# Kernel optimization log

Hardware: AMD Instinct MI355X
Metric: run time of the kernel (lower is better)

## Reference

```python
import jax, jax.numpy as jnp
import numpy as np
import math

D_MODEL = 1024
NHEAD = 16
D_K = D_MODEL // NHEAD
LAMDA_ATT = 1.0
B, L = 2, 2048


def setup_inputs() -> dict:
    key = jax.random.key(0)
    ks = jax.random.split(key, 10)
    s = 1.0 / math.sqrt(D_MODEL)
    x = jax.random.normal(ks[0], (B, L, D_MODEL), dtype=jnp.float32)
    delta_r = jax.random.uniform(ks[1], (B, L), dtype=jnp.float32)  # positive, fed to log
    Wq = jax.random.normal(ks[2], (D_MODEL, D_MODEL), dtype=jnp.float32) * s
    Wk = jax.random.normal(ks[3], (D_MODEL, D_MODEL), dtype=jnp.float32) * s
    Wv = jax.random.normal(ks[4], (D_MODEL, D_MODEL), dtype=jnp.float32) * s
    Wo = jax.random.normal(ks[5], (D_MODEL, D_MODEL), dtype=jnp.float32) * s
    bq = jnp.zeros((D_MODEL,), jnp.float32)
    bk = jnp.zeros((D_MODEL,), jnp.float32)
    bv = jnp.zeros((D_MODEL,), jnp.float32)
    bo = jnp.zeros((D_MODEL,), jnp.float32)
    return {"x": x, "delta_r": delta_r, "Wq": Wq, "bq": bq, "Wk": Wk, "bk": bk,
            "Wv": Wv, "bv": bv, "Wo": Wo, "bo": bo}


def reference(x, delta_r, Wq, bq, Wk, bk, Wv, bv, Wo, bo):
    b, l, d = x.shape
    h, dk = NHEAD, D_K

    def proj(y, W, bias):
        # [B,L,D] -> [B,H,L,dk]
        return (y @ W + bias).reshape(b, l, h, dk).transpose(0, 2, 1, 3)

    v_scaled = x * delta_r[..., None]
    q = proj(x, Wq, bq)
    k = proj(x, Wk, bk)
    v = proj(v_scaled, Wv, bv)

    scores = jnp.einsum('bhqd,bhkd->bhqk', q, k) / math.sqrt(dk)
    pos = jnp.arange(l)
    dist = jnp.abs(pos[None, :] - pos[:, None]).astype(scores.dtype)  # [L,L]
    rel_bias = LAMDA_ATT * jnp.log(delta_r + 1e-6)  # [B,L]
    scores = scores - dist[None, None] * 0.1 + rel_bias[:, None, None, :]

    attn = jax.nn.softmax(scores, axis=-1)  # dropout is identity in eval mode
    context = jnp.einsum('bhqk,bhkd->bqhd', attn, v).reshape(b, l, d)
    out = context @ Wo + bo
    return out, attn.mean(axis=1)
```

## Files before the change

kernel.cpp:

```cpp
#include <hip/hip_runtime.h>
#include <math.h>

#define DMODEL 1024
#define NHEAD  16
#define DK     64
#define BB     2
#define LL     2048
#define MTOT   (BB*LL)

#define LOG2E      1.4426950408889634f
#define SCQ        (0.125f * LOG2E)
#define C2LOG      (0.1f * LOG2E)
#define SKIP_BOUND (-24.0f)

typedef __bf16 bf16_t;
typedef __bf16 bf16x8 __attribute__((ext_vector_type(8)));
typedef __bf16 bf16x4 __attribute__((ext_vector_type(4)));
typedef float  f32x4  __attribute__((ext_vector_type(4)));

static __device__ __forceinline__ f32x4 mfma16(bf16x8 a, bf16x8 b, f32x4 c) {
    return __builtin_amdgcn_mfma_f32_16x16x32_bf16(a, b, c, 0, 0, 0);
}
static __device__ __forceinline__ float exp2f_fast(float x) {
    return __builtin_amdgcn_exp2f(x);
}
static __device__ __forceinline__ float log2f_fast(float x) {
    return __builtin_amdgcn_logf(x);
}
static __device__ __forceinline__ void gl_lds16(const bf16_t* g, bf16_t* l) {
    __builtin_amdgcn_global_load_lds(
        (const __attribute__((address_space(1))) unsigned int*)g,
        (__attribute__((address_space(3))) unsigned int*)l, 16, 0, 0);
}

__global__ __launch_bounds__(256) void prep_fused_k(
    const float* __restrict__ x, const float* __restrict__ dr,
    bf16_t* __restrict__ xb, float* __restrict__ logd2,
    const float* __restrict__ Wq, const float* __restrict__ Wk,
    const float* __restrict__ Wv, const float* __restrict__ Wo,
    bf16_t* __restrict__ Wcat, bf16_t* __restrict__ Wot)
{
    __shared__ __align__(16) float Ts[64][68];
    const int bid = blockIdx.x;
    const int tid = threadIdx.x;
    if (bid < 2048) {
        size_t gid = (size_t)bid * 256 + tid;
        size_t off = gid * 8;
        float4 a = *(const float4*)(x + off);
        float4 c = *(const float4*)(x + off + 4);
        float va[8] = {a.x, a.y, a.z, a.w, c.x, c.y, c.z, c.w};
        bf16x8 o1;
#pragma unroll
        for (int j = 0; j < 8; ++j) o1[j] = (bf16_t)va[j];
        *(bf16x8*)(xb + off) = o1;
        if (gid < MTOT) logd2[gid] = log2f_fast(dr[gid] + 1e-6f);
    } else {
        const int t = bid - 2048;
        const int z = t >> 8;
        const float* W = (z == 0) ? Wq : (z == 1) ? Wk : (z == 2) ? Wv : Wo;
        bf16_t* dst = (z < 3) ? (Wcat + (size_t)z * DMODEL * DMODEL) : Wot;
        const int k0 = (t & 15) * 64, n0 = ((t >> 4) & 15) * 64;
#pragma unroll
        for (int i = 0; i < 4; ++i) {
            int u = tid + 256 * i, r = u >> 4, c4 = (u & 15) * 4;
            *(float4*)&Ts[r][c4] = *(const float4*)(W + (size_t)(k0 + r) * DMODEL + n0 + c4);
        }
        __syncthreads();
#pragma unroll
        for (int i = 0; i < 2; ++i) {
            int u = tid + 256 * i, n = u >> 3, k8 = (u & 7) * 8;
            bf16x8 v;
#pragma unroll
            for (int j = 0; j < 8; ++j) v[j] = (bf16_t)Ts[k8 + j][n];
            *(bf16x8*)(dst + (size_t)(n0 + n) * DMODEL + k0 + k8) = v;
        }
    }
}

__global__ __launch_bounds__(256, 3) void gemm128_k(
    const bf16_t* __restrict__ A, const bf16_t* __restrict__ Bt,
    const float* __restrict__ b0, const float* __restrict__ b1,
    const float* __restrict__ b2, const float* __restrict__ delta,
    bf16_t* __restrict__ outQ, bf16_t* __restrict__ outK,
    bf16_t* __restrict__ outVt)
{
    __shared__ __align__(16) bf16_t Asw[128 * 64];
    __shared__ __align__(16) bf16_t Bsw[128 * 64];
    const int tid = threadIdx.x, lane = tid & 63, w = tid >> 6;
    const int quad = lane >> 4, n16 = lane & 15;
    const int wm = (w & 1) * 64, wn = (w >> 1) * 64;
    const int m0 = blockIdx.y * 128, n0 = blockIdx.x * 128;
    const int srow = lane >> 3;
    const int scb  = (lane & 7) ^ srow;

    f32x4 acc[4][4] = {};

    for (int K0 = 0; K0 < DMODEL; K0 += 64) {
        __syncthreads();
#pragma unroll
        for (int i = 0; i < 4; ++i) {
            int rb = w * 32 + i * 8;
            gl_lds16(A  + (size_t)(m0 + rb + srow) * DMODEL + K0 + scb * 8,
                     &Asw[rb * 64]);
            gl_lds16(Bt + (size_t)(n0 + rb + srow) * DMODEL + K0 + scb * 8,
                     &Bsw[rb * 64]);
        }
        __syncthreads();
#pragma unroll
        for (int kc = 0; kc < 2; ++kc) {
            const int pcb = ((kc * 4 + quad) ^ (n16 & 7)) * 8;
            bf16x8 af[4], bfv[4];
#pragma unroll
            for (int mi = 0; mi < 4; ++mi)
                af[mi] = *(const bf16x8*)&Asw[(wm + mi * 16 + n16) * 64 + pcb];
#pragma unroll
            for (int ni = 0; ni < 4; ++ni)
                bfv[ni] = *(const bf16x8*)&Bsw[(wn + ni * 16 + n16) * 64 + pcb];
#pragma unroll
            for (int mi = 0; mi < 4; ++mi)
#pragma unroll
                for (int ni = 0; ni < 4; ++ni)
                    acc[mi][ni] = mfma16(af[mi], bfv[ni], acc[mi][ni]);
        }
    }

    const int region = n0 >> 10;
    if (region == 2) {
#pragma unroll
        for (int mi = 0; mi < 4; ++mi) {
            const int mbase = m0 + wm + mi * 16 + quad * 4;
            const int bidx = mbase >> 11, l = mbase & (LL - 1);
            const f32x4 dm4 = *(const f32x4*)(delta + mbase);
#pragma unroll
            for (int ni = 0; ni < 4; ++ni) {
                const int nl = (n0 & 1023) + wn + ni * 16 + n16;
                const int h = nl >> 6, dd = nl & 63;
                const float bv = b2[nl];
                bf16x4 pk;
#pragma unroll
                for (int r = 0; r < 4; ++r)
                    pk[r] = (bf16_t)(acc[mi][ni][r] * dm4[r] + bv);
                *(bf16x4*)(outVt + ((size_t)(bidx * NHEAD + h) * DK + dd) * LL + l) = pk;
            }
        }
    } else {
        const float* bias = (region == 0) ? b0 : b1;
        bf16_t* dst = (region == 0) ? outQ : outK;
        const float qs = (region == 0) ? SCQ : 1.0f;
#pragma unroll
        for (int mi = 0; mi < 4; ++mi) {
#pragma unroll
            for (int r = 0; r < 4; ++r) {
                const int m = m0 + wm + mi * 16 + quad * 4 + r;
                const int bidx = m >> 11, l = m & (LL - 1);
#pragma unroll
                for (int ni = 0; ni < 4; ++ni) {
                    const int nl = (n0 & 1023) + wn + ni * 16 + n16;
                    const int h = nl >> 6, dd = nl & 63;
                    float v = (acc[mi][ni][r] + bias[nl]) * qs;
                    dst[(((size_t)(bidx * NHEAD + h) * LL) + l) * DK + dd] = (bf16_t)v;
                }
            }
        }
    }
}

__global__ __launch_bounds__(256) void stats_k(
    const bf16_t* __restrict__ Q, const bf16_t* __restrict__ K,
    const float* __restrict__ logd2, float* __restrict__ Qn,
    float* __restrict__ Kn, float* __restrict__ dlb, float* __restrict__ ldx)
{
    __shared__ float qn_s[256], kn_s[256], dg_s[256];
    const int blk = blockIdx.x;
    const int bh = blk >> 3, seg = blk & 7, b = bh >> 4;
    const int tid = threadIdx.x;
    const int row = seg * 256 + tid;
    const size_t base = (size_t)bh * LL * DK;

    float qn2 = 0.f, kn2 = 0.f, dg = 0.f;
#pragma unroll
    for (int j = 0; j < 8; ++j) {
        bf16x8 qv = *(const bf16x8*)(Q + base + (size_t)row * DK + j * 8);
        bf16x8 kv = *(const bf16x8*)(K + base + (size_t)row * DK + j * 8);
#pragma unroll
        for (int e = 0; e < 8; ++e) {
            float fq = (float)qv[e], fk = (float)kv[e];
            qn2 += fq * fq; kn2 += fk * fk; dg += fq * fk;
        }
    }
    qn_s[tid] = qn2;
    kn_s[tid] = kn2;
    dg_s[tid] = dg + logd2[b * LL + row];
    __syncthreads();

    if (tid < 2) {
        float mq = 0.f, md = 1e30f;
        for (int r = 0; r < 128; ++r) {
            mq = fmaxf(mq, qn_s[tid * 128 + r]);
            md = fminf(md, dg_s[tid * 128 + r]);
        }
        Qn[bh * 16 + seg * 2 + tid] = sqrtf(mq);
        dlb[bh * 16 + seg * 2 + tid] = md;
    } else if (tid >= 64 && tid < 68) {
        const int t = tid - 64;
        float mk = 0.f;
        for (int r = 0; r < 64; ++r) mk = fmaxf(mk, kn_s[t * 64 + r]);
        Kn[bh * 32 + seg * 4 + t] = sqrtf(mk);
    } else if (tid >= 128 && tid < 132 && (bh & 15) == 0) {
        const int t = tid - 128;
        float ml = -1e30f;
        for (int r = 0; r < 64; ++r)
            ml = fmaxf(ml, logd2[b * LL + seg * 256 + t * 64 + r]);
        ldx[b * 32 + seg * 4 + t] = ml;
    }
}

__global__ __launch_bounds__(256, 4) void attn_flash_mfma_k(
    const bf16_t* __restrict__ Q, const bf16_t* __restrict__ K,
    const bf16_t* __restrict__ Vt, const float* __restrict__ logd2,
    const float* __restrict__ Qn, const float* __restrict__ Kn,
    const float* __restrict__ dlb, const float* __restrict__ ldx,
    bf16_t* __restrict__ ctx, float* __restrict__ mlout,
    float* __restrict__ mlmin64)
{
    __shared__ __align__(16) bf16_t Ks[64][64];
    __shared__ __align__(16) bf16_t Vts[64][64];
    __shared__ __align__(16) bf16_t Ps[4][16][72];
    __shared__ float wvmin[4];

    const int tid = threadIdx.x;
    const int lane = tid & 63, w = tid >> 6;
    const int quad = lane >> 4, n16 = lane & 15;
    const int bh = blockIdx.x, b = bh >> 4, h = bh & 15;
    const int qt = blockIdx.y, q0 = qt * 64;
    const size_t base = (size_t)bh * LL * DK;
    const int q = q0 + w * 16 + n16;

    bf16x8 qa[2];
#pragma unroll
    for (int kc = 0; kc < 2; ++kc)
        qa[kc] = *(const bf16x8*)(Q + base + (size_t)q * DK + kc * 32 + quad * 8);

    unsigned mask = 0;
    {
        const float qn = Qn[bh * 16 + (qt >> 1)], dl = dlb[bh * 16 + (qt >> 1)];
        for (int t = 0; t < 32; ++t) {
            const int kc0 = t * 64;
            const int dmin = (kc0 > q0 + 63) ? (kc0 - (q0 + 63))
                           : ((q0 > kc0 + 63) ? (q0 - (kc0 + 63)) : 0);
            const float bound = qn * Kn[bh * 32 + t] + ldx[b * 32 + t]
                              - C2LOG * (float)dmin - dl;
            if (bound > SKIP_BOUND) mask |= (1u << t);
        }
    }

    const int strow = tid >> 3;
    const int sgc   = (tid & 7) ^ (strow & 7);
    const int sdc8  = (tid & 7) * 8;
    bf16x8 kr0, kr1, vr0, vr1;
    auto prefetch = [&](int k0) {
        kr0 = *(const bf16x8*)(K + base + (size_t)(k0 + strow) * DK + sgc * 8);
        kr1 = *(const bf16x8*)(K + base + (size_t)(k0 + 32 + strow) * DK + sgc * 8);
        vr0 = *(const bf16x8*)(Vt + base + (size_t)strow * LL + k0 + sgc * 8);
        vr1 = *(const bf16x8*)(Vt + base + (size_t)(32 + strow) * LL + k0 + sgc * 8);
    };

    float m_c = -1e30f, l_c = 0.f;
    f32x4 o[4] = {};
    const float dfq = (float)(q - quad * 4);

    int t = (int)__builtin_ctz(mask);
    prefetch(t * 64);
    for (;;) {
        const unsigned rem = (t < 31) ? (mask >> (t + 1)) : 0u;
        const int tn = rem ? (t + 1 + (int)__builtin_ctz(rem)) : -1;
        __syncthreads();
        *(bf16x8*)&Ks[strow][sdc8]       = kr0;
        *(bf16x8*)&Ks[32 + strow][sdc8]  = kr1;
        *(bf16x8*)&Vts[strow][sdc8]      = vr0;
        *(bf16x8*)&Vts[32 + strow][sdc8] = vr1;
        __syncthreads();
        if (tn >= 0) prefetch(tn * 64);
        const int k0 = t * 64;

        f32x4 s[4] = {};
#pragma unroll
        for (int kc = 0; kc < 2; ++kc) {
            const int ch = ((kc * 4 + quad) ^ (n16 & 7)) * 8;
#pragma unroll
            for (int kt = 0; kt < 4; ++kt) {
                bf16x8 kb = *(const bf16x8*)&Ks[kt * 16 + n16][ch];
                s[kt] = mfma16(kb, qa[kc], s[kt]);
            }
        }
        const float df = dfq - (float)k0;
#pragma unroll
        for (int kt = 0; kt < 4; ++kt) {
            const f32x4 ldv = *(const f32x4*)(logd2 + b * LL + k0 +
                                              kt * 16 + quad * 4);
#pragma unroll
            for (int r = 0; r < 4; ++r)
                s[kt][r] += ldv[r] - C2LOG * fabsf(df - (float)(kt * 16 + r));
        }
        f32x4 mx;
#pragma unroll
        for (int r = 0; r < 4; ++r)
            mx[r] = fmaxf(fmaxf(s[0][r], s[1][r]), fmaxf(s[2][r], s[3][r]));
        float rm = fmaxf(fmaxf(mx[0], mx[1]), fmaxf(mx[2], mx[3]));
        rm = fmaxf(rm, __shfl_xor(rm, 16));
        rm = fmaxf(rm, __shfl_xor(rm, 32));
        const float mn = fmaxf(m_c, rm);
        const float alpha = exp2f_fast(m_c - mn);
        if (__any(mn > m_c)) {
#pragma unroll
            for (int dt = 0; dt < 4; ++dt)
#pragma unroll
                for (int r = 0; r < 4; ++r) o[dt][r] *= alpha;
        }
        f32x4 ps = {0.f, 0.f, 0.f, 0.f};
#pragma unroll
        for (int kt = 0; kt < 4; ++kt)
#pragma unroll
            for (int r = 0; r < 4; ++r) {
                float p = exp2f_fast(s[kt][r] - mn);
                s[kt][r] = p;
                ps[r] += p;
            }
        float psum = (ps[0] + ps[1]) + (ps[2] + ps[3]);
        psum += __shfl_xor(psum, 16);
        psum += __shfl_xor(psum, 32);
        l_c = l_c * alpha + psum;
        m_c = mn;
#pragma unroll
        for (int kt = 0; kt < 4; ++kt) {
            bf16x4 pk;
#pragma unroll
            for (int r = 0; r < 4; ++r) pk[r] = (bf16_t)s[kt][r];
            *(bf16x4*)&Ps[w][n16][kt * 16 + quad * 4] = pk;
        }
        __threadfence_block();
#pragma unroll
        for (int kc = 0; kc < 2; ++kc) {
            const int ch = ((kc * 4 + quad) ^ (n16 & 7)) * 8;
            bf16x8 pa = *(const bf16x8*)&Ps[w][n16][kc * 32 + quad * 8];
#pragma unroll
            for (int dt = 0; dt < 4; ++dt) {
                bf16x8 vb = *(const bf16x8*)&Vts[dt * 16 + n16][ch];
                o[dt] = mfma16(vb, pa, o[dt]);
            }
        }
        if (tn < 0) break;
        t = tn;
    }
    const float inv = 1.f / l_c;
#pragma unroll
    for (int dt = 0; dt < 4; ++dt) {
        bf16x4 ov;
#pragma unroll
        for (int r = 0; r < 4; ++r) ov[r] = (bf16_t)(o[dt][r] * inv);
        *(bf16x4*)(ctx + ((size_t)b * LL + q) * DMODEL + h * DK +
                   dt * 16 + quad * 4) = ov;
    }
    float mlv = m_c + log2f_fast(l_c);
    if (quad == 0)
        mlout[(size_t)bh * LL + q] = mlv;
    mlv = fminf(mlv, __shfl_xor(mlv, 1));
    mlv = fminf(mlv, __shfl_xor(mlv, 2));
    mlv = fminf(mlv, __shfl_xor(mlv, 4));
    mlv = fminf(mlv, __shfl_xor(mlv, 8));
    if (lane == 0) wvmin[w] = mlv;
    __syncthreads();
    if (tid == 0)
        mlmin64[bh * 32 + qt] = fminf(fminf(wvmin[0], wvmin[1]),
                                      fminf(wvmin[2], wvmin[3]));
}

__global__ __launch_bounds__(256, 3) void tail_fused_k(
    const bf16_t* __restrict__ A, const bf16_t* __restrict__ Bt,
    const float* __restrict__ b0, float* __restrict__ outf,
    const bf16_t* __restrict__ Q, const bf16_t* __restrict__ K,
    const float* __restrict__ logd2, const float* __restrict__ mlws,
    const float* __restrict__ Qn, const float* __restrict__ Kn,
    const float* __restrict__ ml64, const float* __restrict__ ldx,
    float* __restrict__ outmean)
{
    __shared__ __align__(16) char smem[24576];

    const int bid = blockIdx.x;
    const int tid = threadIdx.x;
    const int lane = tid & 63, w = tid >> 6;
    const int quad = lane >> 4, n16 = lane & 15;

    if (bid >= 2048) {
        bf16_t* Asw = (bf16_t*)smem;
        bf16_t* Bsw = (bf16_t*)(smem + 8192);
        const int gb = bid - 2048;
        const int wm = (w & 1) * 32, wn = (w >> 1) * 64;
        const int m0 = (gb >> 3) * 64, n0 = (gb & 7) * 128;
        const int srow = lane >> 3;
        const int scb  = (lane & 7) ^ srow;

        f32x4 acc[2][4] = {};

        for (int K0 = 0; K0 < DMODEL; K0 += 64) {
            __syncthreads();
#pragma unroll
            for (int i = 0; i < 2; ++i) {
                int rb = w * 16 + i * 8;
                gl_lds16(A + (size_t)(m0 + rb + srow) * DMODEL + K0 + scb * 8,
                         &Asw[rb * 64]);
            }
#pragma unroll
            for (int i = 0; i < 4; ++i) {
                int rb = w * 32 + i * 8;
                gl_lds16(Bt + (size_t)(n0 + rb + srow) * DMODEL + K0 + scb * 8,
                         &Bsw[rb * 64]);
            }
            __syncthreads();
#pragma unroll
            for (int kc = 0; kc < 2; ++kc) {
                const int pcb = ((kc * 4 + quad) ^ (n16 & 7)) * 8;
                bf16x8 af[2], bfv[4];
#pragma unroll
                for (int mi = 0; mi < 2; ++mi)
                    af[mi] = *(const bf16x8*)&Asw[(wm + mi * 16 + n16) * 64 + pcb];
#pragma unroll
                for (int ni = 0; ni < 4; ++ni)
                    bfv[ni] = *(const bf16x8*)&Bsw[(wn + ni * 16 + n16) * 64 + pcb];
#pragma unroll
                for (int mi = 0; mi < 2; ++mi)
#pragma unroll
                    for (int ni = 0; ni < 4; ++ni)
                        acc[mi][ni] = mfma16(af[mi], bfv[ni], acc[mi][ni]);
            }
        }
#pragma unroll
        for (int mi = 0; mi < 2; ++mi) {
#pragma unroll
            for (int r = 0; r < 4; ++r) {
                const int m = m0 + wm + mi * 16 + quad * 4 + r;
#pragma unroll
                for (int ni = 0; ni < 4; ++ni) {
                    const int n = n0 + wn + ni * 16 + n16;
                    outf[(size_t)m * DMODEL + n] = acc[mi][ni][r] + b0[n];
                }
            }
        }
        return;
    }

    const int rank = bid >> 6, bq = bid & 63, b = bq >> 5, q64i = bq & 31;
    const int q0 = q64i * 64;

    int ktile = 0;
    {
        const int c = q64i;
        int want = rank;
        for (int d = 0; d < 32; ++d) {
            int ka = c - d;
            if (ka >= 0) {
                if (want == 0) { ktile = ka; break; }
                --want;
            }
            int kb2 = c + d;
            if (d > 0 && kb2 < 32) {
                if (want == 0) { ktile = kb2; break; }
                --want;
            }
        }
    }
    const int k0 = ktile * 64;

    const int qt = q0 >> 7;
    const int qt64 = q0 >> 6;
    const int dmin = (k0 > q0 + 63) ? (k0 - (q0 + 63))
                   : ((q0 > k0 + 63) ? (q0 - (k0 + 63)) : 0);
    unsigned hmask = 0;
    {
        const float dterm = ldx[b * 32 + ktile] - C2LOG * (float)dmin;
        for (int h = 0; h < NHEAD; ++h) {
            const int bh = b * 16 + h;
            const float bound = Qn[bh * 16 + qt] * Kn[bh * 32 + ktile] + dterm
                              - ml64[bh * 32 + qt64];
            if (bound > SKIP_BOUND) hmask |= (1u << h);
        }
    }

    if (!hmask) {
        const int row = tid >> 2, c4 = (tid & 3) * 4;
        const f32x4 z = {0.f, 0.f, 0.f, 0.f};
        float* dst = outmean + ((size_t)b * LL + q0 + row) * LL + k0 + c4;
#pragma unroll
        for (int cc = 0; cc < 4; ++cc)
            *(f32x4*)(dst + cc * 16) = z;
        return;
    }

    typedef bf16_t KsRow2[64][64];
    KsRow2* Ks = (KsRow2*)smem;

    const int qq = q0 + w * 16 + n16;

    float bias0[4][4];
    {
        const float df = (float)(qq - k0 - quad * 4);
#pragma unroll
        for (int kt = 0; kt < 4; ++kt) {
            const f32x4 ldv = *(const f32x4*)(logd2 + b * LL + k0 +
                                              kt * 16 + quad * 4);
#pragma unroll
            for (int r = 0; r < 4; ++r)
                bias0[kt][r] = ldv[r] - C2LOG * fabsf(df - (float)(kt * 16 + r));
        }
    }

    f32x4 acc[4] = {};
    {
        const int strow = tid >> 3;
        const int sgc   = (tid & 7) ^ (strow & 7);
        const int sdc8  = (tid & 7) * 8;
        bf16x8 kr0, kr1, qan[2];
        auto load_head = [&](int h) {
            const size_t hb = (size_t)(b * NHEAD + h) * LL * DK;
            kr0 = *(const bf16x8*)(K + hb + (size_t)(k0 + strow) * DK + sgc * 8);
            kr1 = *(const bf16x8*)(K + hb + (size_t)(k0 + 32 + strow) * DK + sgc * 8);
#pragma unroll
            for (int kc = 0; kc < 2; ++kc)
                qan[kc] = *(const bf16x8*)(Q + hb + (size_t)qq * DK +
                                           kc * 32 + quad * 8);
        };

        int h = (int)__builtin_ctz(hmask);
        load_head(h);
        int pc = 0;
        for (;;) {
            const unsigned rem = (h < 15) ? (hmask >> (h + 1)) : 0u;
            const int hn = rem ? (h + 1 + (int)__builtin_ctz(rem)) : -1;
            const int p = pc & 1;
            *(bf16x8*)&Ks[p][strow][sdc8]      = kr0;
            *(bf16x8*)&Ks[p][32 + strow][sdc8] = kr1;
            bf16x8 qc[2] = {qan[0], qan[1]};
            const float ml = mlws[(size_t)(b * NHEAD + h) * LL + qq];
            __syncthreads();
            if (hn >= 0) load_head(hn);

            f32x4 s[4] = {};
#pragma unroll
            for (int kc = 0; kc < 2; ++kc) {
                const int ch = (((kc * 4 + quad) ^ (n16 & 7))) * 8;
#pragma unroll
                for (int kt = 0; kt < 4; ++kt) {
                    bf16x8 kb = *(const bf16x8*)&Ks[p][kt * 16 + n16][ch];
                    s[kt] = mfma16(kb, qc[kc], s[kt]);
                }
            }
#pragma unroll
            for (int kt = 0; kt < 4; ++kt)
#pragma unroll
                for (int r = 0; r < 4; ++r)
                    acc[kt][r] += exp2f_fast(s[kt][r] + bias0[kt][r] - ml);
            ++pc;
            if (hn < 0) break;
            h = hn;
        }
    }

    const float invH = 1.f / (float)NHEAD;
#pragma unroll
    for (int kt = 0; kt < 4; ++kt) {
        f32x4 ov;
#pragma unroll
        for (int r = 0; r < 4; ++r) ov[r] = acc[kt][r] * invH;
        *(f32x4*)(outmean + ((size_t)b * LL + qq) * LL + k0 +
                  kt * 16 + quad * 4) = ov;
    }
}

extern "C" void kernel_launch(void* const* d_in, const int* in_sizes, int n_in,
                              void* d_out, int out_size, void* d_ws, size_t ws_size,
                              hipStream_t stream) {
    const float* x  = (const float*)d_in[0];
    const float* dr = (const float*)d_in[1];
    const float* Wq = (const float*)d_in[2];
    const float* bq = (const float*)d_in[3];
    const float* Wk = (const float*)d_in[4];
    const float* bk = (const float*)d_in[5];
    const float* Wv = (const float*)d_in[6];
    const float* bv = (const float*)d_in[7];
    const float* Wo = (const float*)d_in[8];
    const float* bo = (const float*)d_in[9];
    float* out = (float*)d_out;
    char* ws = (char*)d_ws;
    const size_t MB = 1ull << 20;

    bf16_t* xb   = (bf16_t*)(ws);
    bf16_t* Wcat = (bf16_t*)(ws + 8 * MB);
    bf16_t* Wot  = (bf16_t*)(ws + 14 * MB);
    bf16_t* Qb   = (bf16_t*)(ws + 16 * MB);
    bf16_t* Kb   = (bf16_t*)(ws + 24 * MB);
    bf16_t* Vtb  = (bf16_t*)(ws + 32 * MB);
    float*  logd = (float*)(ws + 40 * MB);
    float*  mlws = (float*)(ws + 41 * MB);
    float*  Qns  = (float*)(ws + 42 * MB);
    float*  Kns  = (float*)(ws + 42 * MB + 4096);
    float*  dlb  = (float*)(ws + 42 * MB + 12288);
    float*  ldxp = (float*)(ws + 42 * MB + 16384);
    float*  ml64 = (float*)(ws + 42 * MB + 20480);
    bf16_t* ctx  = xb;

    prep_fused_k<<<3072, 256, 0, stream>>>(x, dr, xb, logd,
                                           Wq, Wk, Wv, Wo, Wcat, Wot);

    gemm128_k<<<dim3(24, 32), 256, 0, stream>>>(xb, Wcat, bq, bk, bv, dr,
                                                Qb, Kb, Vtb);
    stats_k<<<256, 256, 0, stream>>>(Qb, Kb, logd, Qns, Kns, dlb, ldxp);

    attn_flash_mfma_k<<<dim3(32, 32), 256, 0, stream>>>(Qb, Kb, Vtb, logd,
                                                        Qns, Kns, dlb, ldxp,
                                                        ctx, mlws, ml64);
    tail_fused_k<<<2560, 256, 0, stream>>>(ctx, Wot, bo, out,
                                           Qb, Kb, logd, mlws, Qns, Kns,
                                           ml64, ldxp,
                                           out + (size_t)MTOT * DMODEL);
}
```

Measured before the change: 213.9 us.

## Process two 64-row query groups per attention block to reuse K/V tiles

Each attention block now handles 128 query rows as two 64-row groups, so every K/V tile staged in shared memory serves twice as many queries. This halves the grid and the global K/V traffic per query, and the skip mask is now computed over a 128-row window. In exchange, per-thread register state doubles, occupancy drops from 4 to 3 blocks per CU, and the coarser skip mask may process tiles that either half alone could skip.

```diff
diff --git a/kernel.cpp b/kernel.cpp
--- a/kernel.cpp
+++ b/kernel.cpp
@@ -215,7 +215,7 @@
     }
 }
 
-__global__ __launch_bounds__(256, 4) void attn_flash_mfma_k(
+__global__ __launch_bounds__(256, 3) void attn_flash_mfma_k(
     const bf16_t* __restrict__ Q, const bf16_t* __restrict__ K,
     const bf16_t* __restrict__ Vt, const float* __restrict__ logd2,
     const float* __restrict__ Qn, const float* __restrict__ Kn,
@@ -226,27 +226,30 @@
     __shared__ __align__(16) bf16_t Ks[64][64];
     __shared__ __align__(16) bf16_t Vts[64][64];
     __shared__ __align__(16) bf16_t Ps[4][16][72];
-    __shared__ float wvmin[4];
+    __shared__ float wvmin[2][4];
 
     const int tid = threadIdx.x;
     const int lane = tid & 63, w = tid >> 6;
     const int quad = lane >> 4, n16 = lane & 15;
     const int bh = blockIdx.x, b = bh >> 4, h = bh & 15;
-    const int qt = blockIdx.y, q0 = qt * 64;
+    const int qt = blockIdx.y, q0 = qt * 128;
     const size_t base = (size_t)bh * LL * DK;
-    const int q = q0 + w * 16 + n16;
-
-    bf16x8 qa[2];
-#pragma unroll
-    for (int kc = 0; kc < 2; ++kc)
-        qa[kc] = *(const bf16x8*)(Q + base + (size_t)q * DK + kc * 32 + quad * 8);
+    const int qr[2] = {q0 + w * 16 + n16, q0 + 64 + w * 16 + n16};
+
+    bf16x8 qa[2][2];
+#pragma unroll
+    for (int qg = 0; qg < 2; ++qg)
+#pragma unroll
+        for (int kc = 0; kc < 2; ++kc)
+            qa[qg][kc] = *(const bf16x8*)(Q + base + (size_t)qr[qg] * DK +
+                                          kc * 32 + quad * 8);
 
     unsigned mask = 0;
     {
-        const float qn = Qn[bh * 16 + (qt >> 1)], dl = dlb[bh * 16 + (qt >> 1)];
+        const float qn = Qn[bh * 16 + qt], dl = dlb[bh * 16 + qt];
         for (int t = 0; t < 32; ++t) {
             const int kc0 = t * 64;
-            const int dmin = (kc0 > q0 + 63) ? (kc0 - (q0 + 63))
+            const int dmin = (kc0 > q0 + 127) ? (kc0 - (q0 + 127))
                            : ((q0 > kc0 + 63) ? (q0 - (kc0 + 63)) : 0);
             const float bound = qn * Kn[bh * 32 + t] + ldx[b * 32 + t]
                               - C2LOG * (float)dmin - dl;
@@ -265,9 +268,8 @@
         vr1 = *(const bf16x8*)(Vt + base + (size_t)(32 + strow) * LL + k0 + sgc * 8);
     };
 
-    float m_c = -1e30f, l_c = 0.f;
-    f32x4 o[4] = {};
-    const float dfq = (float)(q - quad * 4);
+    float m_c[2] = {-1e30f, -1e30f}, l_c[2] = {0.f, 0.f};
+    f32x4 o[2][4] = {};
 
     int t = (int)__builtin_ctz(mask);
     prefetch(t * 64);
@@ -283,96 +285,104 @@
         if (tn >= 0) prefetch(tn * 64);
         const int k0 = t * 64;
 
-        f32x4 s[4] = {};
-#pragma unroll
-        for (int kc = 0; kc < 2; ++kc) {
-            const int ch = ((kc * 4 + quad) ^ (n16 & 7)) * 8;
+#pragma unroll
+        for (int qg = 0; qg < 2; ++qg) {
+            f32x4 s[4] = {};
+#pragma unroll
+            for (int kc = 0; kc < 2; ++kc) {
+                const int ch = ((kc * 4 + quad) ^ (n16 & 7)) * 8;
+#pragma unroll
+                for (int kt = 0; kt < 4; ++kt) {
+                    bf16x8 kb = *(const bf16x8*)&Ks[kt * 16 + n16][ch];
+                    s[kt] = mfma16(kb, qa[qg][kc], s[kt]);
+                }
+            }
+            const float df = (float)(qr[qg] - quad * 4 - k0);
 #pragma unroll
             for (int kt = 0; kt < 4; ++kt) {
-                bf16x8 kb = *(const bf16x8*)&Ks[kt * 16 + n16][ch];
-                s[kt] = mfma16(kb, qa[kc], s[kt]);
-            }
-        }
-        const float df = dfq - (float)k0;
-#pragma unroll
-        for (int kt = 0; kt < 4; ++kt) {
-            const f32x4 ldv = *(const f32x4*)(logd2 + b * LL + k0 +
-                                              kt * 16 + quad * 4);
+                const f32x4 ldv = *(const f32x4*)(logd2 + b * LL + k0 +
+                                                  kt * 16 + quad * 4);
+#pragma unroll
+                for (int r = 0; r < 4; ++r)
+                    s[kt][r] += ldv[r] - C2LOG * fabsf(df - (float)(kt * 16 + r));
+            }
+            f32x4 mx;
 #pragma unroll
             for (int r = 0; r < 4; ++r)
-                s[kt][r] += ldv[r] - C2LOG * fabsf(df - (float)(kt * 16 + r));
-        }
-        f32x4 mx;
-#pragma unroll
-        for (int r = 0; r < 4; ++r)
-            mx[r] = fmaxf(fmaxf(s[0][r], s[1][r]), fmaxf(s[2][r], s[3][r]));
-        float rm = fmaxf(fmaxf(mx[0], mx[1]), fmaxf(mx[2], mx[3]));
-        rm = fmaxf(rm, __shfl_xor(rm, 16));
-        rm = fmaxf(rm, __shfl_xor(rm, 32));
-        const float mn = fmaxf(m_c, rm);
-        const float alpha = exp2f_fast(m_c - mn);
-        if (__any(mn > m_c)) {
-#pragma unroll
-            for (int dt = 0; dt < 4; ++dt)
-#pragma unroll
-                for (int r = 0; r < 4; ++r) o[dt][r] *= alpha;
-        }
-        f32x4 ps = {0.f, 0.f, 0.f, 0.f};
-#pragma unroll
-        for (int kt = 0; kt < 4; ++kt)
-#pragma unroll
-            for (int r = 0; r < 4; ++r) {
-                float p = exp2f_fast(s[kt][r] - mn);
-                s[kt][r] = p;
-                ps[r] += p;
-            }
-        float psum = (ps[0] + ps[1]) + (ps[2] + ps[3]);
-        psum += __shfl_xor(psum, 16);
-        psum += __shfl_xor(psum, 32);
-        l_c = l_c * alpha + psum;
-        m_c = mn;
-#pragma unroll
-        for (int kt = 0; kt < 4; ++kt) {
-            bf16x4 pk;
-#pragma unroll
-            for (int r = 0; r < 4; ++r) pk[r] = (bf16_t)s[kt][r];
-            *(bf16x4*)&Ps[w][n16][kt * 16 + quad * 4] = pk;
-        }
-        __threadfence_block();
-#pragma unroll
-        for (int kc = 0; kc < 2; ++kc) {
-            const int ch = ((kc * 4 + quad) ^ (n16 & 7)) * 8;
-            bf16x8 pa = *(const bf16x8*)&Ps[w][n16][kc * 32 + quad * 8];
-#pragma unroll
-            for (int dt = 0; dt < 4; ++dt) {
-                bf16x8 vb = *(const bf16x8*)&Vts[dt * 16 + n16][ch];
-                o[dt] = mfma16(vb, pa, o[dt]);
-            }
+                mx[r] = fmaxf(fmaxf(s[0][r], s[1][r]), fmaxf(s[2][r], s[3][r]));
+            float rm = fmaxf(fmaxf(mx[0], mx[1]), fmaxf(mx[2], mx[3]));
+            rm = fmaxf(rm, __shfl_xor(rm, 16));
+            rm = fmaxf(rm, __shfl_xor(rm, 32));
+            const float mn = fmaxf(m_c[qg], rm);
+            const float alpha = exp2f_fast(m_c[qg] - mn);
+            if (__any(mn > m_c[qg])) {
+#pragma unroll
+                for (int dt = 0; dt < 4; ++dt)
+#pragma unroll
+                    for (int r = 0; r < 4; ++r) o[qg][dt][r] *= alpha;
+            }
+            f32x4 ps = {0.f, 0.f, 0.f, 0.f};
+#pragma unroll
+            for (int kt = 0; kt < 4; ++kt)
+#pragma unroll
+                for (int r = 0; r < 4; ++r) {
+                    float p = exp2f_fast(s[kt][r] - mn);
+                    s[kt][r] = p;
+                    ps[r] += p;
+                }
+            float psum = (ps[0] + ps[1]) + (ps[2] + ps[3]);
+            psum += __shfl_xor(psum, 16);
+            psum += __shfl_xor(psum, 32);
+            l_c[qg] = l_c[qg] * alpha + psum;
+            m_c[qg] = mn;
+#pragma unroll
+            for (int kt = 0; kt < 4; ++kt) {
+                bf16x4 pk;
+#pragma unroll
+                for (int r = 0; r < 4; ++r) pk[r] = (bf16_t)s[kt][r];
+                *(bf16x4*)&Ps[w][n16][kt * 16 + quad * 4] = pk;
+            }
+            __threadfence_block();
+#pragma unroll
+            for (int kc = 0; kc < 2; ++kc) {
+                const int ch = ((kc * 4 + quad) ^ (n16 & 7)) * 8;
+                bf16x8 pa = *(const bf16x8*)&Ps[w][n16][kc * 32 + quad * 8];
+#pragma unroll
+                for (int dt = 0; dt < 4; ++dt) {
+                    bf16x8 vb = *(const bf16x8*)&Vts[dt * 16 + n16][ch];
+                    o[qg][dt] = mfma16(vb, pa, o[qg][dt]);
+                }
+            }
+            __threadfence_block();
         }
         if (tn < 0) break;
         t = tn;
     }
-    const float inv = 1.f / l_c;
-#pragma unroll
-    for (int dt = 0; dt < 4; ++dt) {
-        bf16x4 ov;
-#pragma unroll
-        for (int r = 0; r < 4; ++r) ov[r] = (bf16_t)(o[dt][r] * inv);
-        *(bf16x4*)(ctx + ((size_t)b * LL + q) * DMODEL + h * DK +
-                   dt * 16 + quad * 4) = ov;
-    }
-    float mlv = m_c + log2f_fast(l_c);
-    if (quad == 0)
-        mlout[(size_t)bh * LL + q] = mlv;
-    mlv = fminf(mlv, __shfl_xor(mlv, 1));
-    mlv = fminf(mlv, __shfl_xor(mlv, 2));
-    mlv = fminf(mlv, __shfl_xor(mlv, 4));
-    mlv = fminf(mlv, __shfl_xor(mlv, 8));
-    if (lane == 0) wvmin[w] = mlv;
+#pragma unroll
+    for (int qg = 0; qg < 2; ++qg) {
+        const float inv = 1.f / l_c[qg];
+#pragma unroll
+        for (int dt = 0; dt < 4; ++dt) {
+            bf16x4 ov;
+#pragma unroll
+            for (int r = 0; r < 4; ++r) ov[r] = (bf16_t)(o[qg][dt][r] * inv);
+            *(bf16x4*)(ctx + ((size_t)b * LL + qr[qg]) * DMODEL + h * DK +
+                       dt * 16 + quad * 4) = ov;
+        }
+        float mlv = m_c[qg] + log2f_fast(l_c[qg]);
+        if (quad == 0)
+            mlout[(size_t)bh * LL + qr[qg]] = mlv;
+        mlv = fminf(mlv, __shfl_xor(mlv, 1));
+        mlv = fminf(mlv, __shfl_xor(mlv, 2));
+        mlv = fminf(mlv, __shfl_xor(mlv, 4));
+        mlv = fminf(mlv, __shfl_xor(mlv, 8));
+        if (lane == 0) wvmin[qg][w] = mlv;
+    }
     __syncthreads();
-    if (tid == 0)
-        mlmin64[bh * 32 + qt] = fminf(fminf(wvmin[0], wvmin[1]),
-                                      fminf(wvmin[2], wvmin[3]));
+    if (tid < 2)
+        mlmin64[bh * 32 + qt * 2 + tid] =
+            fminf(fminf(wvmin[tid][0], wvmin[tid][1]),
+                  fminf(wvmin[tid][2], wvmin[tid][3]));
 }
 
 __global__ __launch_bounds__(256, 3) void tail_fused_k(
@@ -615,7 +625,7 @@
                                                 Qb, Kb, Vtb);
     stats_k<<<256, 256, 0, stream>>>(Qb, Kb, logd, Qns, Kns, dlb, ldxp);
 
-    attn_flash_mfma_k<<<dim3(32, 32), 256, 0, stream>>>(Qb, Kb, Vtb, logd,
+    attn_flash_mfma_k<<<dim3(32, 16), 256, 0, stream>>>(Qb, Kb, Vtb, logd,
                                                         Qns, Kns, dlb, ldxp,
                                                         ctx, mlws, ml64);
     tail_fused_k<<<2560, 256, 0, stream>>>(ctx, Wot, bo, out,
```

Result: slower. 223.0 us (+4.3%).
